# Kernel tuning notes

Hardware: AMD Instinct MI355X
Metric: run time of the kernel (lower is better)

Reference implementation:

```python
import jax, jax.numpy as jnp
import numpy as np

B, N, FD, HD, MD, FS, NM = 8, 64, 128, 256, 64, 80, 6
D = HD + MD  # 320: GNN/decoder operating dim (fixes dim bug in original)
H = W = 128

def _mlp2(x, W1, b1, W2, b2):
    return jax.nn.relu(jax.nn.relu(x @ W1 + b1) @ W2 + b2)

def _forward(object_features, object_attributes, perception_features, object_positions,
             enc_W1, enc_b1, enc_W2, enc_b2, conv1_W, conv1_b, conv2_W, conv2_b,
             edge_W1, edge_b1, edge_W2, edge_b2, gru_Wih, gru_Whh, gru_bih, gru_bhh,
             mode_W1, mode_b1, mode_W2, mode_b2, traj_W1, traj_b1, traj_W2, traj_b2):
    # object encoder: [B,N,FD+8] -> [B,N,HD]
    obj_in = jnp.concatenate([object_features, object_attributes], -1)
    emb = _mlp2(obj_in, enc_W1, enc_b1, enc_W2, enc_b2)
    # map encoder (original discards result via random sampler; kept for faithfulness)
    dn = ('NCHW', 'OIHW', 'NCHW')
    m = jax.nn.relu(jax.lax.conv_general_dilated(perception_features, conv1_W, (1, 1), 'SAME', dimension_numbers=dn) + conv1_b[None, :, None, None])
    m = jax.nn.relu(jax.lax.conv_general_dilated(m, conv2_W, (1, 1), 'SAME', dimension_numbers=dn) + conv2_b[None, :, None, None])
    # sample_map_at_positions returns randn in the original; fixed-seed equivalent
    sampled = jax.random.normal(jax.random.key(42), (B, N, MD), dtype=emb.dtype)
    ctx = jnp.concatenate([emb, sampled], -1)  # [B,N,D]
    # Social GNN, fully vectorized over the ego-node loop i:
    rel = object_positions[:, :, None, :] - object_positions[:, None, :, :]  # [B,N,N,2] = pos[i]-pos[j]
    ego = jnp.broadcast_to(ctx[:, :, None, :], (B, N, N, D))
    nbr = jnp.broadcast_to(ctx[:, None, :, :], (B, N, N, D))
    e = _mlp2(jnp.concatenate([ego, nbr, rel], -1), edge_W1, edge_b1, edge_W2, edge_b2)  # [B,N,N,D]
    mask = (1.0 - jnp.eye(N, dtype=e.dtype))[None, :, :, None]
    agg = (e * mask).sum(2) / (N - 1 + 1e-10)  # [B,N,D]
    # GRUCell(input=concat(ctx,agg), hidden=ctx), torch semantics
    x = jnp.concatenate([ctx, agg], -1)  # [B,N,2D]
    gi = x @ gru_Wih + gru_bih
    gh = ctx @ gru_Whh + gru_bhh
    ir, iz, inn = jnp.split(gi, 3, -1)
    hr, hz, hn = jnp.split(gh, 3, -1)
    r = jax.nn.sigmoid(ir + hr)
    z = jax.nn.sigmoid(iz + hz)
    n = jnp.tanh(inn + r * hn)
    h = (1.0 - z) * n + z * ctx  # [B,N,D]
    # multi-modal trajectory decoder
    mode_probs = jax.nn.softmax(jax.nn.relu(h @ mode_W1 + mode_b1) @ mode_W2 + mode_b2, -1)  # [B,N,NM]
    t = jax.nn.relu(jnp.einsum('bnd,mde->bnme', h, traj_W1) + traj_b1)  # [B,N,NM,D]
    traj = jnp.einsum('bnme,mef->bnmf', t, traj_W2) + traj_b2  # [B,N,NM,FS*2]
    traj = traj.reshape(B, N, NM, FS, 2)
    return traj, mode_probs

def setup_inputs() -> dict:
    key = jax.random.key(0)
    ks = jax.random.split(key, 24)
    p = lambda k, shape: jax.random.normal(k, shape, dtype=jnp.float32) * 0.02
    z = lambda *shape: jnp.zeros(shape, dtype=jnp.float32)
    return {
        'object_features': jax.random.normal(ks[0], (B, N, FD), dtype=jnp.float32),
        'object_attributes': jax.random.normal(ks[1], (B, N, 8), dtype=jnp.float32),
        'perception_features': jax.random.normal(ks[2], (B, 256, H, W), dtype=jnp.float32),
        'object_positions': jax.random.normal(ks[3], (B, N, 2), dtype=jnp.float32),
        'enc_W1': p(ks[4], (FD + 8, HD)), 'enc_b1': z(HD),
        'enc_W2': p(ks[5], (HD, HD)), 'enc_b2': z(HD),
        'conv1_W': p(ks[6], (128, 256, 3, 3)), 'conv1_b': z(128),
        'conv2_W': p(ks[7], (64, 128, 3, 3)), 'conv2_b': z(64),
        'edge_W1': p(ks[8], (2 * D + 2, D)), 'edge_b1': z(D),
        'edge_W2': p(ks[9], (D, D)), 'edge_b2': z(D),
        'gru_Wih': p(ks[10], (2 * D, 3 * D)), 'gru_Whh': p(ks[11], (D, 3 * D)),
        'gru_bih': z(3 * D), 'gru_bhh': z(3 * D),
        'mode_W1': p(ks[12], (D, D)), 'mode_b1': z(D),
        'mode_W2': p(ks[13], (D, NM)), 'mode_b2': z(NM),
        'traj_W1': p(ks[14], (NM, D, D)), 'traj_b1': z(NM, D),
        'traj_W2': p(ks[15], (NM, D, FS * 2)), 'traj_b2': z(NM, FS * 2),
    }

def reference(object_features, object_attributes, perception_features, object_positions,
              enc_W1, enc_b1, enc_W2, enc_b2, conv1_W, conv1_b, conv2_W, conv2_b,
              edge_W1, edge_b1, edge_W2, edge_b2, gru_Wih, gru_Whh, gru_bih, gru_bhh,
              mode_W1, mode_b1, mode_W2, mode_b2, traj_W1, traj_b1, traj_W2, traj_b2):
    return _forward(object_features, object_attributes, perception_features, object_positions,
                    enc_W1, enc_b1, enc_W2, enc_b2, conv1_W, conv1_b, conv2_W, conv2_b,
                    edge_W1, edge_b1, edge_W2, edge_b2, gru_Wih, gru_Whh, gru_bih, gru_bhh,
                    mode_W1, mode_b1, mode_W2, mode_b2, traj_W1, traj_b1, traj_W2, traj_b2)
```

## Files before the change

### kernel.cpp

```cpp
#include <hip/hip_runtime.h>


typedef __attribute__((ext_vector_type(8))) short bf16x8;
typedef __attribute__((ext_vector_type(4))) float f32x4;

__device__ __forceinline__ unsigned short f2bf(float x) {
  unsigned u = __float_as_uint(x);
  return (unsigned short)((u + 0x7fffu + ((u >> 16) & 1u)) >> 16);
}

__device__ __forceinline__ void threefry2x32(unsigned k0, unsigned k1,
                                             unsigned& x0, unsigned& x1) {
  const unsigned ks0 = k0, ks1 = k1, ks2 = k0 ^ k1 ^ 0x1BD11BDAu;
  x0 += ks0; x1 += ks1;
#define TFR(r) { x0 += x1; x1 = (x1 << (r)) | (x1 >> (32 - (r))); x1 ^= x0; }
  TFR(13) TFR(15) TFR(26) TFR(6)  x0 += ks1; x1 += ks2 + 1u;
  TFR(17) TFR(29) TFR(16) TFR(24) x0 += ks2; x1 += ks0 + 2u;
  TFR(13) TFR(15) TFR(26) TFR(6)  x0 += ks0; x1 += ks1 + 3u;
  TFR(17) TFR(29) TFR(16) TFR(24) x0 += ks1; x1 += ks2 + 4u;
  TFR(13) TFR(15) TFR(26) TFR(6)  x0 += ks2; x1 += ks0 + 5u;
#undef TFR
}

__device__ __forceinline__ float erfinv_xla(float x) {
  float w = -logf((1.0f - x) * (1.0f + x));
  float p;
  if (w < 5.0f) {
    w = w - 2.5f;
    p = 2.81022636e-08f;
    p = fmaf(p, w, 3.43273939e-07f);
    p = fmaf(p, w, -3.5233877e-06f);
    p = fmaf(p, w, -4.39150654e-06f);
    p = fmaf(p, w, 0.00021858087f);
    p = fmaf(p, w, -0.00125372503f);
    p = fmaf(p, w, -0.00417768164f);
    p = fmaf(p, w, 0.246640727f);
    p = fmaf(p, w, 1.50140941f);
  } else {
    w = sqrtf(w) - 3.0f;
    p = -0.000200214257f;
    p = fmaf(p, w, 0.000100950558f);
    p = fmaf(p, w, 0.00134934322f);
    p = fmaf(p, w, -0.00367342844f);
    p = fmaf(p, w, 0.00573950773f);
    p = fmaf(p, w, -0.0076224613f);
    p = fmaf(p, w, 0.00943887047f);
    p = fmaf(p, w, 1.00167406f);
    p = fmaf(p, w, 2.83297682f);
  }
  return p * x;
}

__device__ __forceinline__ float jax_normal42(unsigned idx) {
  unsigned x0 = 0u, x1 = idx;
  threefry2x32(0u, 42u, x0, x1);
  unsigned bits = x0 ^ x1;
  float f = __uint_as_float((bits >> 9) | 0x3f800000u) - 1.0f;
  const float lo = -0.99999994f;
  float u = fmaxf(lo, f * 2.0f + lo);
  return 1.41421356237f * erfinv_xla(u);
}

__device__ __forceinline__ void cvt_octet(const float* __restrict__ src,
                                          unsigned short* __restrict__ dst,
                                          int rem, int N) {
  const int g = rem / N, n = rem - g * N;
  const float* s = src + g * 8 * N + n;
  unsigned short v[8];
#pragma unroll
  for (int e = 0; e < 8; ++e) v[e] = f2bf(s[e * N]);
  ushort4* d = (ushort4*)&dst[(size_t)rem * 8];
  d[0] = make_ushort4(v[0], v[1], v[2], v[3]);
  d[1] = make_ushort4(v[4], v[5], v[6], v[7]);
}

__global__ __launch_bounds__(256)
void k_head(const float* __restrict__ feat, const float* __restrict__ attr,
            const float* __restrict__ eW1, const float* __restrict__ eb1,
            const float* __restrict__ eW2, const float* __restrict__ eb2,
            float* __restrict__ ctx,
            const float* __restrict__ W2e, const float* __restrict__ EW1,
            unsigned short* __restrict__ ub) {
  __shared__ float s_in[4][136];
  __shared__ float s_h1[4][256];
  const int t = threadIdx.x;

  if (blockIdx.x >= 128) {
    const int id = (blockIdx.x - 128) * 256 + t;
    if (id < 12800)      cvt_octet(W2e, ub, id, 320);
    else if (id < 38400) cvt_octet(EW1, ub + 1945600, id - 12800, 320);
    return;
  }

  const int r0 = blockIdx.x * 4;
  for (int r = 0; r < 4; ++r) {
    if (t < 128)      s_in[r][t] = feat[(r0 + r) * 128 + t];
    else if (t < 136) s_in[r][t] = attr[(r0 + r) * 8 + (t - 128)];
  }
  __syncthreads();
  float acc[4];
#pragma unroll
  for (int r = 0; r < 4; ++r) acc[r] = eb1[t];
  for (int k = 0; k < 136; ++k) {
    const float w = eW1[k * 256 + t];
#pragma unroll
    for (int r = 0; r < 4; ++r) acc[r] = fmaf(s_in[r][k], w, acc[r]);
  }
#pragma unroll
  for (int r = 0; r < 4; ++r) s_h1[r][t] = fmaxf(acc[r], 0.0f);
  __syncthreads();
#pragma unroll
  for (int r = 0; r < 4; ++r) acc[r] = eb2[t];
  for (int k = 0; k < 256; ++k) {
    const float w = eW2[k * 256 + t];
#pragma unroll
    for (int r = 0; r < 4; ++r) acc[r] = fmaf(s_h1[r][k], w, acc[r]);
  }
#pragma unroll
  for (int r = 0; r < 4; ++r) ctx[(r0 + r) * 320 + t] = fmaxf(acc[r], 0.0f);
  if (t < 64) {
    for (int r = 0; r < 4; ++r)
      ctx[(r0 + r) * 320 + 256 + t] = jax_normal42((unsigned)((r0 + r) * 64 + t));
  }
}

__global__ __launch_bounds__(256)
void k_pqM(const float* __restrict__ ctx, const unsigned short* __restrict__ Bf,
           const float* __restrict__ b1, float* __restrict__ P,
           float* __restrict__ Q, const float* __restrict__ Wih,
           const float* __restrict__ Whh, unsigned short* __restrict__ ub) {
  __shared__ __align__(16) unsigned short s_c[40 * 16 * 8];
  const int t = threadIdx.x;

  if (blockIdx.x >= 64) {
    const int id = (blockIdx.x - 64) * 256 + t;
    if (id < 76800)       cvt_octet(Wih, ub + 102400, id, 960);
    else if (id < 115200) cvt_octet(Whh, ub + 716800, id - 76800, 960);
    return;
  }

  const int row0 = (blockIdx.x >> 1) * 16;
  const int half = blockIdx.x & 1;
#pragma unroll
  for (int it = 0; it < 3; ++it) {
    const int idx = t + it * 256;
    if (idx < 640) {
      const int row = idx / 40, oct = idx - row * 40;
      const float4 v0 = *(const float4*)&ctx[(row0 + row) * 320 + oct * 8];
      const float4 v1 = *(const float4*)&ctx[(row0 + row) * 320 + oct * 8 + 4];
      ushort4* dst = (ushort4*)&s_c[(oct * 16 + row) * 8];
      dst[0] = make_ushort4(f2bf(v0.x), f2bf(v0.y), f2bf(v0.z), f2bf(v0.w));
      dst[1] = make_ushort4(f2bf(v1.x), f2bf(v1.y), f2bf(v1.z), f2bf(v1.w));
    }
  }
  __syncthreads();

  const int w = t >> 6, l = t & 63, lg = l >> 4, lr = l & 15;
  f32x4 acc[5];
#pragma unroll
  for (int u = 0; u < 5; ++u) acc[u] = (f32x4){0.f, 0.f, 0.f, 0.f};
#pragma unroll
  for (int ks = 0; ks < 10; ++ks) {
    const bf16x8 afr = *(const bf16x8*)&s_c[((ks * 4 + lg) * 16 + lr) * 8];
    bf16x8 bfr[5];
#pragma unroll
    for (int u = 0; u < 5; ++u)
      bfr[u] = *(const bf16x8*)&Bf[(((ks * 4 + lg) * 640) + half * 320 +
                                    w * 80 + u * 16 + lr) * 8];
#pragma unroll
    for (int u = 0; u < 5; ++u)
      acc[u] = __builtin_amdgcn_mfma_f32_16x16x32_bf16(afr, bfr[u], acc[u], 0, 0, 0);
  }
#pragma unroll
  for (int u = 0; u < 5; ++u) {
    const int n = w * 80 + u * 16 + lr;
    const float bias = (half == 0) ? b1[n] : 0.0f;
    float* dst = (half == 0) ? P : Q;
#pragma unroll
    for (int r = 0; r < 4; ++r) {
      const int row = row0 + lg * 4 + r;
      dst[row * 320 + n] = acc[u][r] + bias;
    }
  }
}

__global__ __launch_bounds__(256)
void k_edge(const float* __restrict__ P, const float* __restrict__ Q,
            const float* __restrict__ pos, const float* __restrict__ W1,
            const unsigned short* __restrict__ Bf, const float* __restrict__ b2,
            float* __restrict__ agg,
            const float* __restrict__ T1, const float* __restrict__ T2,
            const float* __restrict__ MW1, const float* __restrict__ MW2,
            unsigned short* __restrict__ ub) {
  __shared__ __align__(16) unsigned short s_A[40 * 64 * 8];
  const int t = threadIdx.x;

  if (blockIdx.x >= 512) {
    const int id = (blockIdx.x - 512) * 256 + t;
    if (id >= 128640) return;
    if (id >= 128000) {
      const int rem = id - 128000;
      const int g = rem >> 4, n = rem & 15;
      unsigned short v[8];
#pragma unroll
      for (int e = 0; e < 8; ++e) v[e] = (n < 6) ? f2bf(MW2[(g * 8 + e) * 6 + n]) : 0;
      ushort4* d = (ushort4*)&ub[2252800 + (size_t)rem * 8];
      d[0] = make_ushort4(v[0], v[1], v[2], v[3]);
      d[1] = make_ushort4(v[4], v[5], v[6], v[7]);
      return;
    }
    if (id < 76800)       cvt_octet(T1, ub + 1024000, id, 320);
    else if (id < 115200) cvt_octet(T2, ub + 1638400, id - 76800, 160);
    else                  cvt_octet(MW1, ub + 2150400, id - 115200, 320);
    return;
  }

  const int bx = blockIdx.x;
  const int b = bx >> 6, i = bx & 63;
  const int w = t >> 6, l = t & 63;

  {
    const float2 pi = *(const float2*)&pos[b * 128 + 2 * i];
    const float* __restrict__ Prow = P + bx * 320;
    const float* __restrict__ w0 = W1 + 640 * 320;
    const float* __restrict__ w1 = W1 + 641 * 320;
#pragma unroll
    for (int it = 0; it < 10; ++it) {
      const int tau = w * 640 + it * 64 + l;
      const int j = tau / 40;
      const int oct = tau - j * 40;
      const int k0 = oct * 8;
      const float2 pj = *(const float2*)&pos[b * 128 + 2 * j];
      const float rx = pi.x - pj.x, ry = pi.y - pj.y;
      const float* __restrict__ Qrow = Q + (b * 64 + j) * 320;
      const float4 q0 = *(const float4*)&Qrow[k0];
      const float4 q1 = *(const float4*)&Qrow[k0 + 4];
      const float4 p0 = *(const float4*)&Prow[k0];
      const float4 p1 = *(const float4*)&Prow[k0 + 4];
      const float4 a0 = *(const float4*)&w0[k0];
      const float4 a1 = *(const float4*)&w0[k0 + 4];
      const float4 c0 = *(const float4*)&w1[k0];
      const float4 c1 = *(const float4*)&w1[k0 + 4];
      float v[8];
      v[0] = fmaf(ry, c0.x, fmaf(rx, a0.x, p0.x + q0.x));
      v[1] = fmaf(ry, c0.y, fmaf(rx, a0.y, p0.y + q0.y));
      v[2] = fmaf(ry, c0.z, fmaf(rx, a0.z, p0.z + q0.z));
      v[3] = fmaf(ry, c0.w, fmaf(rx, a0.w, p0.w + q0.w));
      v[4] = fmaf(ry, c1.x, fmaf(rx, a1.x, p1.x + q1.x));
      v[5] = fmaf(ry, c1.y, fmaf(rx, a1.y, p1.y + q1.y));
      v[6] = fmaf(ry, c1.z, fmaf(rx, a1.z, p1.z + q1.z));
      v[7] = fmaf(ry, c1.w, fmaf(rx, a1.w, p1.w + q1.w));
      unsigned short u[8];
#pragma unroll
      for (int e = 0; e < 8; ++e) u[e] = f2bf(fmaxf(v[e], 0.0f));
      const int swz = ((oct * 64 + j) * 8) ^ ((oct & 7) << 3);
      *(ushort4*)&s_A[swz]     = make_ushort4(u[0], u[1], u[2], u[3]);
      *(ushort4*)&s_A[swz + 4] = make_ushort4(u[4], u[5], u[6], u[7]);
    }
  }
  __syncthreads();

  f32x4 acc[4][5];
#pragma unroll
  for (int mt = 0; mt < 4; ++mt)
#pragma unroll
    for (int u = 0; u < 5; ++u) acc[mt][u] = (f32x4){0.f, 0.f, 0.f, 0.f};

  const int lg = l >> 4, lr = l & 15;
  const unsigned short* __restrict__ Bbase = Bf + (lg * 320 + w * 80 + lr) * 8;

#pragma unroll 2
  for (int ks = 0; ks < 10; ++ks) {
    const int oct = ks * 4 + lg;
    bf16x8 afr[4];
#pragma unroll
    for (int mt = 0; mt < 4; ++mt) {
      const int elem = ((oct * 64 + mt * 16 + lr) * 8) ^ ((oct & 7) << 3);
      afr[mt] = *(const bf16x8*)&s_A[elem];
    }
    bf16x8 bfr[5];
#pragma unroll
    for (int u = 0; u < 5; ++u)
      bfr[u] = *(const bf16x8*)(Bbase + ks * 10240 + u * 128);
#pragma unroll
    for (int mt = 0; mt < 4; ++mt)
#pragma unroll
      for (int u = 0; u < 5; ++u)
        acc[mt][u] = __builtin_amdgcn_mfma_f32_16x16x32_bf16(
            afr[mt], bfr[u], acc[mt][u], 0, 0, 0);
  }

#pragma unroll
  for (int u = 0; u < 5; ++u) {
    const int n = w * 80 + u * 16 + lr;
    const float bias = b2[n];
    float p = 0.0f;
#pragma unroll
    for (int mt = 0; mt < 4; ++mt) {
#pragma unroll
      for (int r = 0; r < 4; ++r) {
        const int j = mt * 16 + lg * 4 + r;
        const float e = fmaxf(acc[mt][u][r] + bias, 0.0f);
        p += (j != i) ? e : 0.0f;
      }
    }
    p += __shfl_xor(p, 16);
    p += __shfl_xor(p, 32);
    if (l < 16) agg[bx * 320 + n] = p * (1.0f / 63.0f);
  }
}

__global__ __launch_bounds__(256)
void k_gruM(const float* __restrict__ ctx, const float* __restrict__ agg,
            const unsigned short* __restrict__ BfI,
            const unsigned short* __restrict__ BfH,
            const float* __restrict__ bih, const float* __restrict__ bhh,
            float* __restrict__ h) {
  __shared__ __align__(16) unsigned short s_x[80 * 16 * 8];
  const int rb = blockIdx.x / 5, db = blockIdx.x % 5;
  const int row0 = rb * 16, d0 = db * 64;
  const int t = threadIdx.x;

#pragma unroll
  for (int it = 0; it < 5; ++it) {
    const int idx = t + it * 256;
    const int row = idx / 80, oct = idx - row * 80;
    float4 v0, v1;
    if (oct < 40) {
      v0 = *(const float4*)&ctx[(row0 + row) * 320 + oct * 8];
      v1 = *(const float4*)&ctx[(row0 + row) * 320 + oct * 8 + 4];
    } else {
      v0 = *(const float4*)&agg[(row0 + row) * 320 + (oct - 40) * 8];
      v1 = *(const float4*)&agg[(row0 + row) * 320 + (oct - 40) * 8 + 4];
    }
    ushort4* dst = (ushort4*)&s_x[(oct * 16 + row) * 8];
    dst[0] = make_ushort4(f2bf(v0.x), f2bf(v0.y), f2bf(v0.z), f2bf(v0.w));
    dst[1] = make_ushort4(f2bf(v1.x), f2bf(v1.y), f2bf(v1.z), f2bf(v1.w));
  }
  __syncthreads();

  const int w = t >> 6, l = t & 63, lg = l >> 4, lr = l & 15;
  const int d = d0 + w * 16 + lr;

  f32x4 accI[3], accH[3];
#pragma unroll
  for (int g = 0; g < 3; ++g) {
    accI[g] = (f32x4){0.f, 0.f, 0.f, 0.f};
    accH[g] = (f32x4){0.f, 0.f, 0.f, 0.f};
  }

#pragma unroll 2
  for (int ks = 0; ks < 20; ++ks) {
    const bf16x8 afr = *(const bf16x8*)&s_x[((ks * 4 + lg) * 16 + lr) * 8];
    bf16x8 bfr[3];
#pragma unroll
    for (int g = 0; g < 3; ++g)
      bfr[g] = *(const bf16x8*)&BfI[((ks * 4 + lg) * 960 + g * 320 + d) * 8];
#pragma unroll
    for (int g = 0; g < 3; ++g)
      accI[g] = __builtin_amdgcn_mfma_f32_16x16x32_bf16(afr, bfr[g], accI[g], 0, 0, 0);
  }
#pragma unroll 2
  for (int ks = 0; ks < 10; ++ks) {
    const bf16x8 afr = *(const bf16x8*)&s_x[((ks * 4 + lg) * 16 + lr) * 8];
    bf16x8 bfr[3];
#pragma unroll
    for (int g = 0; g < 3; ++g)
      bfr[g] = *(const bf16x8*)&BfH[((ks * 4 + lg) * 960 + g * 320 + d) * 8];
#pragma unroll
    for (int g = 0; g < 3; ++g)
      accH[g] = __builtin_amdgcn_mfma_f32_16x16x32_bf16(afr, bfr[g], accH[g], 0, 0, 0);
  }

  const float b_ir = bih[d], b_iz = bih[320 + d], b_in = bih[640 + d];
  const float b_hr = bhh[d], b_hz = bhh[320 + d], b_hn = bhh[640 + d];
#pragma unroll
  for (int r = 0; r < 4; ++r) {
    const int row = row0 + lg * 4 + r;
    const float ir = accI[0][r] + b_ir;
    const float iz = accI[1][r] + b_iz;
    const float inn = accI[2][r] + b_in;
    const float hr = accH[0][r] + b_hr;
    const float hz = accH[1][r] + b_hz;
    const float hn = accH[2][r] + b_hn;
    const float rr = 1.0f / (1.0f + expf(-(ir + hr)));
    const float zz = 1.0f / (1.0f + expf(-(iz + hz)));
    const float nn = tanhf(fmaf(rr, hn, inn));
    const float c = ctx[row * 320 + d];
    h[row * 320 + d] = (1.0f - zz) * nn + zz * c;
  }
}

__global__ __launch_bounds__(256)
void k_tail(const float* __restrict__ h, const unsigned short* __restrict__ MB1,
            const float* __restrict__ mb1, const unsigned short* __restrict__ MB2,
            const float* __restrict__ mb2, const unsigned short* __restrict__ TB1,
            const float* __restrict__ tb1, const unsigned short* __restrict__ TB2,
            const float* __restrict__ tb2, float* __restrict__ out) {
  __shared__ __align__(16) unsigned short s_buf[20480];
  __shared__ float s_l[32][6];
  const int t = threadIdx.x;
  const int w = t >> 6, l = t & 63, lg = l >> 4, lr = l & 15;

  if (blockIdx.x < 16) {
    unsigned short* s_h = s_buf;
    unsigned short* s_t = s_buf + 10240;
    const int row0 = blockIdx.x * 32;
#pragma unroll
    for (int it = 0; it < 5; ++it) {
      const int idx = t + it * 256;
      const int row = idx / 40, oct = idx - row * 40;
      const float4 v0 = *(const float4*)&h[(row0 + row) * 320 + oct * 8];
      const float4 v1 = *(const float4*)&h[(row0 + row) * 320 + oct * 8 + 4];
      ushort4* dst = (ushort4*)&s_h[(oct * 32 + row) * 8];
      dst[0] = make_ushort4(f2bf(v0.x), f2bf(v0.y), f2bf(v0.z), f2bf(v0.w));
      dst[1] = make_ushort4(f2bf(v1.x), f2bf(v1.y), f2bf(v1.z), f2bf(v1.w));
    }
    __syncthreads();

    f32x4 acc1[2][5];
#pragma unroll
    for (int mt = 0; mt < 2; ++mt)
#pragma unroll
      for (int u = 0; u < 5; ++u) acc1[mt][u] = (f32x4){0.f, 0.f, 0.f, 0.f};
#pragma unroll
    for (int ks = 0; ks < 10; ++ks) {
      bf16x8 afr[2];
#pragma unroll
      for (int mt = 0; mt < 2; ++mt)
        afr[mt] = *(const bf16x8*)&s_h[(((ks * 4 + lg) * 32) + mt * 16 + lr) * 8];
      bf16x8 bfr[5];
#pragma unroll
      for (int u = 0; u < 5; ++u)
        bfr[u] = *(const bf16x8*)&MB1[((ks * 4 + lg) * 320 + w * 80 + u * 16 + lr) * 8];
#pragma unroll
      for (int mt = 0; mt < 2; ++mt)
#pragma unroll
        for (int u = 0; u < 5; ++u)
          acc1[mt][u] = __builtin_amdgcn_mfma_f32_16x16x32_bf16(
              afr[mt], bfr[u], acc1[mt][u], 0, 0, 0);
    }
#pragma unroll
    for (int u = 0; u < 5; ++u) {
      const int n = w * 80 + u * 16 + lr;
      const float bias = mb1[n];
#pragma unroll
      for (int mt = 0; mt < 2; ++mt) {
#pragma unroll
        for (int r = 0; r < 4; ++r) {
          const int row = mt * 16 + lg * 4 + r;
          s_t[((n >> 3) * 32 + row) * 8 + (n & 7)] =
              f2bf(fmaxf(acc1[mt][u][r] + bias, 0.0f));
        }
      }
    }
    __syncthreads();

    if (w < 2) {
      f32x4 acc2 = (f32x4){0.f, 0.f, 0.f, 0.f};
#pragma unroll
      for (int ks = 0; ks < 10; ++ks) {
        const bf16x8 afr = *(const bf16x8*)&s_t[(((ks * 4 + lg) * 32) + w * 16 + lr) * 8];
        const bf16x8 bfr = *(const bf16x8*)&MB2[((ks * 4 + lg) * 16 + lr) * 8];
        acc2 = __builtin_amdgcn_mfma_f32_16x16x32_bf16(afr, bfr, acc2, 0, 0, 0);
      }
      if (lr < 6) {
#pragma unroll
        for (int r = 0; r < 4; ++r)
          s_l[w * 16 + lg * 4 + r][lr] = acc2[r] + mb2[lr];
      }
    }
    __syncthreads();

    if (t < 32) {
      float v[6];
#pragma unroll
      for (int q = 0; q < 6; ++q) v[q] = s_l[t][q];
      float mx = v[0];
#pragma unroll
      for (int q = 1; q < 6; ++q) mx = fmaxf(mx, v[q]);
      float sum = 0.0f;
#pragma unroll
      for (int q = 0; q < 6; ++q) { v[q] = expf(v[q] - mx); sum += v[q]; }
      const float inv = 1.0f / sum;
#pragma unroll
      for (int q = 0; q < 6; ++q) out[491520 + (row0 + t) * 6 + q] = v[q] * inv;
    }
    return;
  }

  const int idx0 = blockIdx.x - 16;
  const int m = idx0 >> 5, rb = idx0 & 31;
  unsigned short* s_h = s_buf;
  unsigned short* s_t = s_buf + 5120;
  const int row0 = rb * 16;

#pragma unroll
  for (int it = 0; it < 3; ++it) {
    const int idx = t + it * 256;
    if (idx < 640) {
      const int row = idx / 40, oct = idx - row * 40;
      const float4 v0 = *(const float4*)&h[(row0 + row) * 320 + oct * 8];
      const float4 v1 = *(const float4*)&h[(row0 + row) * 320 + oct * 8 + 4];
      ushort4* dst = (ushort4*)&s_h[(oct * 16 + row) * 8];
      dst[0] = make_ushort4(f2bf(v0.x), f2bf(v0.y), f2bf(v0.z), f2bf(v0.w));
      dst[1] = make_ushort4(f2bf(v1.x), f2bf(v1.y), f2bf(v1.z), f2bf(v1.w));
    }
  }
  __syncthreads();

  f32x4 acc1[5];
#pragma unroll
  for (int u = 0; u < 5; ++u) acc1[u] = (f32x4){0.f, 0.f, 0.f, 0.f};
  const unsigned short* __restrict__ B1m = TB1 + m * 102400;
#pragma unroll
  for (int ks = 0; ks < 10; ++ks) {
    const bf16x8 afr = *(const bf16x8*)&s_h[((ks * 4 + lg) * 16 + lr) * 8];
    bf16x8 bfr[5];
#pragma unroll
    for (int u = 0; u < 5; ++u)
      bfr[u] = *(const bf16x8*)&B1m[((ks * 4 + lg) * 320 + w * 80 + u * 16 + lr) * 8];
#pragma unroll
    for (int u = 0; u < 5; ++u)
      acc1[u] = __builtin_amdgcn_mfma_f32_16x16x32_bf16(afr, bfr[u], acc1[u], 0, 0, 0);
  }
#pragma unroll
  for (int u = 0; u < 5; ++u) {
    const int n = w * 80 + u * 16 + lr;
    const float bias = tb1[m * 320 + n];
#pragma unroll
    for (int r = 0; r < 4; ++r) {
      const int row = lg * 4 + r;
      s_t[((n >> 3) * 16 + row) * 8 + (n & 7)] =
          f2bf(fmaxf(acc1[u][r] + bias, 0.0f));
    }
  }
  __syncthreads();

  const int nb = (w == 0) ? 0 : (w == 1) ? 3 : (w == 2) ? 6 : 7;
  f32x4 acc2[3];
#pragma unroll
  for (int u = 0; u < 3; ++u) acc2[u] = (f32x4){0.f, 0.f, 0.f, 0.f};
  const unsigned short* __restrict__ B2m = TB2 + m * 51200;
#pragma unroll
  for (int ks = 0; ks < 10; ++ks) {
    const bf16x8 afr = *(const bf16x8*)&s_t[((ks * 4 + lg) * 16 + lr) * 8];
    bf16x8 bfr[3];
#pragma unroll
    for (int u = 0; u < 3; ++u)
      bfr[u] = *(const bf16x8*)&B2m[((ks * 4 + lg) * 160 + (nb + u) * 16 + lr) * 8];
#pragma unroll
    for (int u = 0; u < 3; ++u)
      acc2[u] = __builtin_amdgcn_mfma_f32_16x16x32_bf16(afr, bfr[u], acc2[u], 0, 0, 0);
  }
#pragma unroll
  for (int u = 0; u < 3; ++u) {
    const int n = (nb + u) * 16 + lr;
    const float bias = tb2[m * 160 + n];
#pragma unroll
    for (int r = 0; r < 4; ++r) {
      const int row = row0 + lg * 4 + r;
      out[(row * 6 + m) * 160 + n] = acc2[u][r] + bias;
    }
  }
}

extern "C" void kernel_launch(void* const* d_in, const int* in_sizes, int n_in,
                              void* d_out, int out_size, void* d_ws, size_t ws_size,
                              hipStream_t stream) {
  (void)in_sizes; (void)n_in; (void)out_size; (void)ws_size;
  const float* feat  = (const float*)d_in[0];
  const float* attr  = (const float*)d_in[1];
  const float* pos   = (const float*)d_in[3];
  const float* encW1 = (const float*)d_in[4];
  const float* encb1 = (const float*)d_in[5];
  const float* encW2 = (const float*)d_in[6];
  const float* encb2 = (const float*)d_in[7];
  const float* edgW1 = (const float*)d_in[12];
  const float* edgb1 = (const float*)d_in[13];
  const float* edgW2 = (const float*)d_in[14];
  const float* edgb2 = (const float*)d_in[15];
  const float* Wih   = (const float*)d_in[16];
  const float* Whh   = (const float*)d_in[17];
  const float* bih   = (const float*)d_in[18];
  const float* bhh   = (const float*)d_in[19];
  const float* mW1   = (const float*)d_in[20];
  const float* mb1   = (const float*)d_in[21];
  const float* mW2   = (const float*)d_in[22];
  const float* mb2   = (const float*)d_in[23];
  const float* tW1   = (const float*)d_in[24];
  const float* tb1   = (const float*)d_in[25];
  const float* tW2   = (const float*)d_in[26];
  const float* tb2   = (const float*)d_in[27];

  float* out = (float*)d_out;
  float* ws  = (float*)d_ws;
  float* ctx  = ws;
  float* P    = ws + 163840;
  float* Q    = ws + 327680;
  float* agg  = ws + 491520;
  float* hbuf = ws + 655360;
  unsigned short* ub = (unsigned short*)(ws + 819200);
  unsigned short* W2bf  = ub;
  unsigned short* WihBf = ub + 102400;
  unsigned short* WhhBf = ub + 716800;
  unsigned short* T1bf  = ub + 1024000;
  unsigned short* T2bf  = ub + 1638400;
  unsigned short* EW1bf = ub + 1945600;
  unsigned short* MW1bf = ub + 2150400;
  unsigned short* MW2bf = ub + 2252800;

  k_head<<<278, 256, 0, stream>>>(feat, attr, encW1, encb1, encW2, encb2, ctx,
                                  edgW2, edgW1, ub);
  k_pqM<<<514, 256, 0, stream>>>(ctx, EW1bf, edgb1, P, Q, Wih, Whh, ub);
  k_edge<<<1015, 256, 0, stream>>>(P, Q, pos, edgW1, W2bf, edgb2, agg,
                                   tW1, tW2, mW1, mW2, ub);
  k_gruM<<<160, 256, 0, stream>>>(ctx, agg, WihBf, WhhBf, bih, bhh, hbuf);
  k_tail<<<208, 256, 0, stream>>>(hbuf, MW1bf, mb1, MW2bf, mb2,
                                  T1bf, tb1, T2bf, tb2, out);
}
```

Measured before the change: 78.82 us.

## Fuse object encoder with edge P/Q projection into one kernel

Merges the encoder MLP kernel and the P/Q projection kernel into a single launch. Each block pair now recomputes the 4-row encoder output, writes ctx from one half only, and feeds bf16 ctx straight into the MFMA projection, reading the fp32 edge W1 and converting it on the fly instead of using a pre-converted bf16 copy. Shared inputs are stored transposed so the inner loops can use float4 loads. The aim is to drop a launch and a ctx round trip through global memory. In exchange, the encoder work is done twice, each MFMA tile uses only 4 of its 16 rows, and B-fragment loads become strided scalar fp32 reads.

```diff
diff --git a/kernel.cpp b/kernel.cpp
--- a/kernel.cpp
+++ b/kernel.cpp
@@ -75,111 +75,125 @@
 }
 
 __global__ __launch_bounds__(256)
-void k_head(const float* __restrict__ feat, const float* __restrict__ attr,
-            const float* __restrict__ eW1, const float* __restrict__ eb1,
-            const float* __restrict__ eW2, const float* __restrict__ eb2,
-            float* __restrict__ ctx,
-            const float* __restrict__ W2e, const float* __restrict__ EW1,
-            unsigned short* __restrict__ ub) {
-  __shared__ float s_in[4][136];
-  __shared__ float s_h1[4][256];
+void k_encpq(const float* __restrict__ feat, const float* __restrict__ attr,
+             const float* __restrict__ eW1, const float* __restrict__ eb1,
+             const float* __restrict__ eW2, const float* __restrict__ eb2,
+             const float* __restrict__ EW1, const float* __restrict__ edgb1,
+             float* __restrict__ ctx, float* __restrict__ P,
+             float* __restrict__ Q,
+             const float* __restrict__ W2e, const float* __restrict__ Wih,
+             const float* __restrict__ Whh, unsigned short* __restrict__ ub) {
+  __shared__ __align__(16) unsigned char smem[10240];
   const int t = threadIdx.x;
 
-  if (blockIdx.x >= 128) {
-    const int id = (blockIdx.x - 128) * 256 + t;
-    if (id < 12800)      cvt_octet(W2e, ub, id, 320);
-    else if (id < 38400) cvt_octet(EW1, ub + 1945600, id - 12800, 320);
+  if (blockIdx.x >= 256) {
+    const int cid = (blockIdx.x - 256) * 256 + t;
+    if (cid < 12800)      cvt_octet(W2e, ub, cid, 320);
+    else if (cid < 89600) cvt_octet(Wih, ub + 102400, cid - 12800, 960);
+    else                  cvt_octet(Whh, ub + 716800, cid - 89600, 960);
     return;
   }
 
-  const int r0 = blockIdx.x * 4;
-  for (int r = 0; r < 4; ++r) {
-    if (t < 128)      s_in[r][t] = feat[(r0 + r) * 128 + t];
-    else if (t < 136) s_in[r][t] = attr[(r0 + r) * 8 + (t - 128)];
+  const int rg = blockIdx.x >> 1;
+  const int half = blockIdx.x & 1;
+  const int r0 = rg * 4;
+
+  float (*s_inT)[4] = (float (*)[4])smem;
+  float (*s_h1T)[4] = (float (*)[4])(smem + 2176);
+#pragma unroll
+  for (int it = 0; it < 3; ++it) {
+    const int idx = t + it * 256;
+    if (idx < 544) {
+      const int k = idx >> 2, r = idx & 3;
+      s_inT[k][r] = (k < 128) ? feat[(r0 + r) * 128 + k]
+                              : attr[(r0 + r) * 8 + (k - 128)];
+    }
   }
   __syncthreads();
   float acc[4];
 #pragma unroll
   for (int r = 0; r < 4; ++r) acc[r] = eb1[t];
   for (int k = 0; k < 136; ++k) {
-    const float w = eW1[k * 256 + t];
-#pragma unroll
-    for (int r = 0; r < 4; ++r) acc[r] = fmaf(s_in[r][k], w, acc[r]);
-  }
-#pragma unroll
-  for (int r = 0; r < 4; ++r) s_h1[r][t] = fmaxf(acc[r], 0.0f);
+    const float ww = eW1[k * 256 + t];
+    const float4 sv = *(const float4*)&s_inT[k][0];
+    acc[0] = fmaf(sv.x, ww, acc[0]);
+    acc[1] = fmaf(sv.y, ww, acc[1]);
+    acc[2] = fmaf(sv.z, ww, acc[2]);
+    acc[3] = fmaf(sv.w, ww, acc[3]);
+  }
+  {
+    float4 h1;
+    h1.x = fmaxf(acc[0], 0.0f); h1.y = fmaxf(acc[1], 0.0f);
+    h1.z = fmaxf(acc[2], 0.0f); h1.w = fmaxf(acc[3], 0.0f);
+    *(float4*)&s_h1T[t][0] = h1;
+  }
   __syncthreads();
 #pragma unroll
   for (int r = 0; r < 4; ++r) acc[r] = eb2[t];
   for (int k = 0; k < 256; ++k) {
-    const float w = eW2[k * 256 + t];
-#pragma unroll
-    for (int r = 0; r < 4; ++r) acc[r] = fmaf(s_h1[r][k], w, acc[r]);
-  }
-#pragma unroll
-  for (int r = 0; r < 4; ++r) ctx[(r0 + r) * 320 + t] = fmaxf(acc[r], 0.0f);
+    const float ww = eW2[k * 256 + t];
+    const float4 sv = *(const float4*)&s_h1T[k][0];
+    acc[0] = fmaf(sv.x, ww, acc[0]);
+    acc[1] = fmaf(sv.y, ww, acc[1]);
+    acc[2] = fmaf(sv.z, ww, acc[2]);
+    acc[3] = fmaf(sv.w, ww, acc[3]);
+  }
+  float smp[4];
   if (t < 64) {
+#pragma unroll
     for (int r = 0; r < 4; ++r)
-      ctx[(r0 + r) * 320 + 256 + t] = jax_normal42((unsigned)((r0 + r) * 64 + t));
-  }
-}
-
-__global__ __launch_bounds__(256)
-void k_pqM(const float* __restrict__ ctx, const unsigned short* __restrict__ Bf,
-           const float* __restrict__ b1, float* __restrict__ P,
-           float* __restrict__ Q, const float* __restrict__ Wih,
-           const float* __restrict__ Whh, unsigned short* __restrict__ ub) {
-  __shared__ __align__(16) unsigned short s_c[40 * 16 * 8];
-  const int t = threadIdx.x;
-
-  if (blockIdx.x >= 64) {
-    const int id = (blockIdx.x - 64) * 256 + t;
-    if (id < 76800)       cvt_octet(Wih, ub + 102400, id, 960);
-    else if (id < 115200) cvt_octet(Whh, ub + 716800, id - 76800, 960);
-    return;
-  }
-
-  const int row0 = (blockIdx.x >> 1) * 16;
-  const int half = blockIdx.x & 1;
-#pragma unroll
-  for (int it = 0; it < 3; ++it) {
-    const int idx = t + it * 256;
-    if (idx < 640) {
-      const int row = idx / 40, oct = idx - row * 40;
-      const float4 v0 = *(const float4*)&ctx[(row0 + row) * 320 + oct * 8];
-      const float4 v1 = *(const float4*)&ctx[(row0 + row) * 320 + oct * 8 + 4];
-      ushort4* dst = (ushort4*)&s_c[(oct * 16 + row) * 8];
-      dst[0] = make_ushort4(f2bf(v0.x), f2bf(v0.y), f2bf(v0.z), f2bf(v0.w));
-      dst[1] = make_ushort4(f2bf(v1.x), f2bf(v1.y), f2bf(v1.z), f2bf(v1.w));
+      smp[r] = jax_normal42((unsigned)((r0 + r) * 64 + t));
+  }
+  __syncthreads();
+
+  unsigned short* s_c = (unsigned short*)smem;
+  {
+    const int oct = t >> 3, e = t & 7;
+#pragma unroll
+    for (int r = 0; r < 4; ++r) {
+      const float v = fmaxf(acc[r], 0.0f);
+      s_c[(oct * 16 + r) * 8 + e] = f2bf(v);
+      if (half == 0) ctx[(r0 + r) * 320 + t] = v;
+    }
+  }
+  if (t < 64) {
+    const int oct = 32 + (t >> 3), e = t & 7;
+#pragma unroll
+    for (int r = 0; r < 4; ++r) {
+      s_c[(oct * 16 + r) * 8 + e] = f2bf(smp[r]);
+      if (half == 0) ctx[(r0 + r) * 320 + 256 + t] = smp[r];
     }
   }
   __syncthreads();
 
   const int w = t >> 6, l = t & 63, lg = l >> 4, lr = l & 15;
-  f32x4 acc[5];
-#pragma unroll
-  for (int u = 0; u < 5; ++u) acc[u] = (f32x4){0.f, 0.f, 0.f, 0.f};
+  f32x4 acc5[5];
+#pragma unroll
+  for (int u = 0; u < 5; ++u) acc5[u] = (f32x4){0.f, 0.f, 0.f, 0.f};
+  const float* __restrict__ Bb = EW1 + 2560 * half + w * 80 + lr;
 #pragma unroll
   for (int ks = 0; ks < 10; ++ks) {
-    const bf16x8 afr = *(const bf16x8*)&s_c[((ks * 4 + lg) * 16 + lr) * 8];
-    bf16x8 bfr[5];
-#pragma unroll
-    for (int u = 0; u < 5; ++u)
-      bfr[u] = *(const bf16x8*)&Bf[(((ks * 4 + lg) * 640) + half * 320 +
-                                    w * 80 + u * 16 + lr) * 8];
-#pragma unroll
-    for (int u = 0; u < 5; ++u)
-      acc[u] = __builtin_amdgcn_mfma_f32_16x16x32_bf16(afr, bfr[u], acc[u], 0, 0, 0);
-  }
+    const int M = ks * 4 + lg;
+    const bf16x8 afr = *(const bf16x8*)&s_c[(M * 16 + lr) * 8];
+    const float* __restrict__ Bm = Bb + 5120 * M;
+#pragma unroll
+    for (int u = 0; u < 5; ++u) {
+      const float* __restrict__ src = Bm + u * 16;
+      bf16x8 bfr;
+#pragma unroll
+      for (int e = 0; e < 8; ++e) bfr[e] = (short)f2bf(src[320 * e]);
+      acc5[u] = __builtin_amdgcn_mfma_f32_16x16x32_bf16(afr, bfr, acc5[u], 0, 0, 0);
+    }
+  }
+  float* __restrict__ dst = half ? Q : P;
 #pragma unroll
   for (int u = 0; u < 5; ++u) {
     const int n = w * 80 + u * 16 + lr;
-    const float bias = (half == 0) ? b1[n] : 0.0f;
-    float* dst = (half == 0) ? P : Q;
+    const float bias = half ? 0.0f : edgb1[n];
 #pragma unroll
     for (int r = 0; r < 4; ++r) {
-      const int row = row0 + lg * 4 + r;
-      dst[row * 320 + n] = acc[u][r] + bias;
+      const int row = lg * 4 + r;
+      if (row < 4) dst[(r0 + row) * 320 + n] = acc5[u][r] + bias;
     }
   }
 }
@@ -606,13 +620,12 @@
   unsigned short* WhhBf = ub + 716800;
   unsigned short* T1bf  = ub + 1024000;
   unsigned short* T2bf  = ub + 1638400;
-  unsigned short* EW1bf = ub + 1945600;
   unsigned short* MW1bf = ub + 2150400;
   unsigned short* MW2bf = ub + 2252800;
 
-  k_head<<<278, 256, 0, stream>>>(feat, attr, encW1, encb1, encW2, encb2, ctx,
-                                  edgW2, edgW1, ub);
-  k_pqM<<<514, 256, 0, stream>>>(ctx, EW1bf, edgb1, P, Q, Wih, Whh, ub);
+  k_encpq<<<756, 256, 0, stream>>>(feat, attr, encW1, encb1, encW2, encb2,
+                                   edgW1, edgb1, ctx, P, Q,
+                                   edgW2, Wih, Whh, ub);
   k_edge<<<1015, 256, 0, stream>>>(P, Q, pos, edgW1, W2bf, edgb2, agg,
                                    tW1, tW2, mW1, mW2, ub);
   k_gruM<<<160, 256, 0, stream>>>(ctx, agg, WihBf, WhhBf, bih, bhh, hbuf);
```

Measured after the change: 79.30 us. No clear change (+0.6%).
